# Performance work log

Hardware: AMD Instinct MI355X
Metric: run time of the kernel (lower is better)

The kernel has to match this reference:

```python
import jax, jax.numpy as jnp
import numpy as np

N = 50000      # nodes
E = 800000     # edges
IN = 128       # in_feats
HID = 16       # h_feats (per head)
HEADS = 8      # num_heads layer 1
CLS = 40       # num_classes
NEG_SLOPE = 0.2


def setup_inputs() -> dict:
    key = jax.random.key(0)
    ks = jax.random.split(key, 12)
    s = lambda fan: np.float32(1.0 / np.sqrt(fan))
    return {
        "features": jax.random.normal(ks[0], (N, IN), jnp.float32),
        "edge_src": jax.random.randint(ks[1], (E,), 0, N, dtype=jnp.int32),
        "edge_dst": jax.random.randint(ks[2], (E,), 0, N, dtype=jnp.int32),
        # layer 1 params
        "W1": jax.random.normal(ks[3], (IN, HEADS * HID), jnp.float32) * s(IN),
        "al1": jax.random.normal(ks[4], (HEADS, HID), jnp.float32) * s(HID),
        "ar1": jax.random.normal(ks[5], (HEADS, HID), jnp.float32) * s(HID),
        "b1": jnp.zeros((HEADS * HID,), jnp.float32),
        # layer 2 params (1 head)
        "W2": jax.random.normal(ks[6], (HEADS * HID, CLS), jnp.float32) * s(HEADS * HID),
        "al2": jax.random.normal(ks[7], (1, CLS), jnp.float32) * s(CLS),
        "ar2": jax.random.normal(ks[8], (1, CLS), jnp.float32) * s(CLS),
        "b2": jnp.zeros((CLS,), jnp.float32),
    }


def gat_conv(x, W, al, ar, b, src, dst, heads, out_dim):
    # x: [N, F_in] -> feat: [N, H, D]
    feat = (x @ W).reshape(-1, heads, out_dim)
    el = (feat * al).sum(-1)                      # [N, H]
    er = (feat * ar).sum(-1)                      # [N, H]
    e = jax.nn.leaky_relu(el[src] + er[dst], NEG_SLOPE)  # [E, H]
    # segment softmax over destination neighborhoods
    emax = jax.ops.segment_max(e, dst, num_segments=N)   # [N, H]
    emax = jnp.where(jnp.isfinite(emax), emax, jnp.float32(0.0))
    ee = jnp.exp(e - emax[dst])                   # [E, H]
    denom = jax.ops.segment_sum(ee, dst, num_segments=N)
    alpha = ee / (denom[dst] + jnp.float32(1e-9)) # [E, H]
    msg = alpha[:, :, None] * feat[src]           # [E, H, D]
    out = jax.ops.segment_sum(msg, dst, num_segments=N)  # [N, H, D]
    return out + b.reshape(1, heads, out_dim)


def reference(features, edge_src, edge_dst, W1, al1, ar1, b1, W2, al2, ar2, b2):
    h = jax.nn.elu(gat_conv(features, W1, al1, ar1, b1, edge_src, edge_dst, HEADS, HID))
    h = h.reshape(N, HEADS * HID)                 # flatten(1)
    out = gat_conv(h, W2, al2, ar2, b2, edge_src, edge_dst, 1, CLS)
    return out.mean(axis=1)                       # [N, CLS]
```

## Files before the change

kernel.cpp:

```cpp
#include <hip/hip_runtime.h>
#include <hip/hip_bf16.h>

#define N_NODES 50000
#define N_EDGES 800000
#define IN_F    128
#define HID     16
#define HEADS   8
#define F1      128
#define CLS     40
#define CLSP    64
#define NEG     0.2f
#define NEG_INF (-__builtin_inff())
#define SWEEPS      8
#define SWEEP_RANGE 6250
#define STRIDE      96

typedef __bf16 bf16x8 __attribute__((ext_vector_type(8)));
typedef float  f32x4  __attribute__((ext_vector_type(4)));
typedef float  f32x2  __attribute__((ext_vector_type(2)));

__device__ __forceinline__ float leaky(float v) { return v >= 0.0f ? v : NEG * v; }
__device__ __forceinline__ f32x2 unpk(unsigned u) {
    f32x2 r;
    r.x = __uint_as_float(u << 16);
    r.y = __uint_as_float(u & 0xffff0000u);
    return r;
}

__global__ void setup_kernel(const float* __restrict__ W1, const float* __restrict__ W2,
                             __bf16* __restrict__ w1t, __bf16* __restrict__ w2t,
                             int* __restrict__ cursor) {
    int i = blockIdx.x * blockDim.x + threadIdx.x;
    if (i < N_NODES) cursor[i] = 0;
    if (i < 128 * 128) {
        int n = i >> 7, k = i & 127;
        w1t[i] = (__bf16)W1[k * 128 + n];
    }
    if (i < CLSP * 128) {
        int n = i >> 7, k = i & 127;
        w2t[i] = (n < CLS) ? (__bf16)W2[k * CLS + n] : (__bf16)0.0f;
    }
}

__global__ void scatter_kernel(const int* __restrict__ src, const int* __restrict__ dst,
                               int* __restrict__ cursor, int* __restrict__ srcs_sorted) {
    const int BPS = (N_EDGES + 255) / 256;
    int sweep = blockIdx.x / BPS;
    int e = (blockIdx.x - sweep * BPS) * 256 + threadIdx.x;
    if (e >= N_EDGES) return;
    int d = dst[e];
    int lo = sweep * SWEEP_RANGE;
    if (d < lo || d >= lo + SWEEP_RANGE) return;
    int pos = d * STRIDE + atomicAdd(&cursor[d], 1);
    srcs_sorted[pos] = src[e];
}

__global__ __launch_bounds__(256) void gemm1_mfma(const float* __restrict__ A,
                                                  const __bf16* __restrict__ Wt,
                                                  const float* __restrict__ al1,
                                                  const float* __restrict__ ar1,
                                                  __bf16* __restrict__ outb,
                                                  float* __restrict__ el,
                                                  float* __restrict__ er) {
    int wave = threadIdx.x >> 6, lane = threadIdx.x & 63;
    int m0 = blockIdx.x * 64 + wave * 16;
    int c = lane & 15;
    int row = m0 + c;
    int rowc = row < N_NODES ? row : N_NODES - 1;
    int ko = (lane >> 4) * 8;

    f32x4 acc[8];
    #pragma unroll
    for (int t = 0; t < 8; ++t)
        #pragma unroll
        for (int r = 0; r < 4; ++r) acc[t][r] = 0.f;

    for (int ks = 0; ks < 128; ks += 32) {
        const float* ap = A + (size_t)rowc * 128 + ks + ko;
        float4 u = *(const float4*)ap;
        float4 v = *(const float4*)(ap + 4);
        bf16x8 a;
        a[0] = (__bf16)u.x; a[1] = (__bf16)u.y; a[2] = (__bf16)u.z; a[3] = (__bf16)u.w;
        a[4] = (__bf16)v.x; a[5] = (__bf16)v.y; a[6] = (__bf16)v.z; a[7] = (__bf16)v.w;
        #pragma unroll
        for (int t = 0; t < 8; ++t) {
            bf16x8 b = *(const bf16x8*)(Wt + (size_t)(t * 16 + c) * 128 + ks + ko);
            acc[t] = __builtin_amdgcn_mfma_f32_16x16x32_bf16(a, b, acc[t], 0, 0, 0);
        }
    }
    int rbase = m0 + (lane >> 4) * 4;
    #pragma unroll
    for (int t = 0; t < 8; ++t) {
        int gcol = t * 16 + c;
        #pragma unroll
        for (int r = 0; r < 4; ++r) {
            int grow = rbase + r;
            if (grow < N_NODES) outb[(size_t)grow * 128 + gcol] = (__bf16)acc[t][r];
        }
    }
    #pragma unroll
    for (int t = 0; t < 8; ++t) {
        float alv = al1[t * 16 + c];
        float arv = ar1[t * 16 + c];
        float pe[4], pr[4];
        #pragma unroll
        for (int r = 0; r < 4; ++r) { pe[r] = acc[t][r] * alv; pr[r] = acc[t][r] * arv; }
        #pragma unroll
        for (int mask = 1; mask <= 8; mask <<= 1) {
            #pragma unroll
            for (int r = 0; r < 4; ++r) {
                pe[r] += __shfl_xor(pe[r], mask, 64);
                pr[r] += __shfl_xor(pr[r], mask, 64);
            }
        }
        if (c == 0) {
            #pragma unroll
            for (int r = 0; r < 4; ++r) {
                int grow = rbase + r;
                if (grow < N_NODES) {
                    el[grow * 8 + t] = pe[r];
                    er[grow * 8 + t] = pr[r];
                }
            }
        }
    }
}

__global__ __launch_bounds__(256) void gemm2_mfma(const __bf16* __restrict__ A,
                                                  const __bf16* __restrict__ Wt,
                                                  const float* __restrict__ al2,
                                                  const float* __restrict__ ar2,
                                                  __bf16* __restrict__ out,
                                                  float* __restrict__ el,
                                                  float* __restrict__ er) {
    int wave = threadIdx.x >> 6, lane = threadIdx.x & 63;
    int m0 = blockIdx.x * 64 + wave * 16;
    int c = lane & 15;
    int row = m0 + c;
    int rowc = row < N_NODES ? row : N_NODES - 1;
    int ko = (lane >> 4) * 8;

    f32x4 acc[4];
    #pragma unroll
    for (int t = 0; t < 4; ++t)
        #pragma unroll
        for (int r = 0; r < 4; ++r) acc[t][r] = 0.f;

    for (int ks = 0; ks < 128; ks += 32) {
        bf16x8 a = *(const bf16x8*)(A + (size_t)rowc * 128 + ks + ko);
        #pragma unroll
        for (int t = 0; t < 4; ++t) {
            bf16x8 b = *(const bf16x8*)(Wt + (size_t)(t * 16 + c) * 128 + ks + ko);
            acc[t] = __builtin_amdgcn_mfma_f32_16x16x32_bf16(a, b, acc[t], 0, 0, 0);
        }
    }
    int rbase = m0 + (lane >> 4) * 4;
    #pragma unroll
    for (int t = 0; t < 4; ++t) {
        int gcol = t * 16 + c;
        #pragma unroll
        for (int r = 0; r < 4; ++r) {
            int grow = rbase + r;
            if (grow < N_NODES) out[(size_t)grow * CLSP + gcol] = (__bf16)acc[t][r];
        }
    }
    float pe[4] = {0.f, 0.f, 0.f, 0.f}, pr[4] = {0.f, 0.f, 0.f, 0.f};
    #pragma unroll
    for (int t = 0; t < 3; ++t) {
        int idx = t * 16 + c;
        float alv = (idx < CLS) ? al2[idx] : 0.f;
        float arv = (idx < CLS) ? ar2[idx] : 0.f;
        #pragma unroll
        for (int r = 0; r < 4; ++r) { pe[r] += acc[t][r] * alv; pr[r] += acc[t][r] * arv; }
    }
    #pragma unroll
    for (int mask = 1; mask <= 8; mask <<= 1) {
        #pragma unroll
        for (int r = 0; r < 4; ++r) {
            pe[r] += __shfl_xor(pe[r], mask, 64);
            pr[r] += __shfl_xor(pr[r], mask, 64);
        }
    }
    if (c == 0) {
        #pragma unroll
        for (int r = 0; r < 4; ++r) {
            int grow = rbase + r;
            if (grow < N_NODES) { el[grow] = pe[r]; er[grow] = pr[r]; }
        }
    }
}

__global__ __launch_bounds__(256) void gat1_fused(const int* __restrict__ degs,
                                                  const int* __restrict__ srcs,
                                                  const float* __restrict__ el,
                                                  const float* __restrict__ er,
                                                  const __bf16* __restrict__ feat1b,
                                                  const float* __restrict__ b1,
                                                  __bf16* __restrict__ hbufb) {
    __shared__ float a_lds[4][64 * 8];
    __shared__ int   s_lds[4][64];
    int wave = threadIdx.x >> 6;
    int lane = threadIdx.x & 63;
    int d = blockIdx.x * 4 + wave;
    int off = d * STRIDE;
    int deg = degs[d];

    int h = lane & 7, slot = lane >> 3;
    int q = lane >> 4, fg = lane & 15, hd = fg >> 1;
    float er_d = er[d * 8 + h];

    f32x2 accv[4];
    #pragma unroll
    for (int j = 0; j < 4; ++j) { accv[j].x = 0.f; accv[j].y = 0.f; }

    bool fast = (deg <= 64);
    if (fast) {
        int nit = (deg + 7) >> 3;
        float sc[8];
        int sreg[8];
        float m = NEG_INF;
        #pragma unroll
        for (int it = 0; it < 8; ++it) {
            float v = NEG_INF;
            int e = it * 8 + slot;
            if (it < nit && e < deg) {
                sreg[it] = srcs[off + e];
                v = leaky(el[sreg[it] * 8 + h] + er_d);
            }
            sc[it] = v;
            m = fmaxf(m, v);
        }
        float l = 0.f;
        #pragma unroll
        for (int it = 0; it < 8; ++it)
            l += (sc[it] == NEG_INF) ? 0.f : __expf(sc[it] - m);
        #pragma unroll
        for (int mask = 8; mask <= 32; mask <<= 1) {
            float m2 = __shfl_xor(m, mask, 64);
            float l2 = __shfl_xor(l, mask, 64);
            float mn = fmaxf(m, m2);
            float f1 = (m  == NEG_INF) ? 0.f : __expf(m - mn);
            float f2 = (m2 == NEG_INF) ? 0.f : __expf(m2 - mn);
            l = l * f1 + l2 * f2;
            m = mn;
        }
        float inv_l = 1.f / (l + 1e-9f);
        #pragma unroll
        for (int it = 0; it < 8; ++it) {
            int e = it * 8 + slot;
            if (it < nit && e < deg) {
                a_lds[wave][e * 8 + h] = __expf(sc[it] - m) * inv_l;
                if (h == 0) s_lds[wave][e] = sreg[it];
            }
        }
    }
    __syncthreads();

    if (fast) {
        int ng = (deg + 3) >> 2;
        #pragma unroll 4
        for (int g = 0; g < ng; ++g) {
            int k = g * 4 + q;
            float a = 0.f;
            int se = 0;
            if (k < deg) {
                a = a_lds[wave][k * 8 + hd];
                se = s_lds[wave][k];
            }
            uint4 p = *(const uint4*)(feat1b + (size_t)se * F1 + fg * 8);
            f32x2 av; av.x = a; av.y = a;
            accv[0] += av * unpk(p.x);
            accv[1] += av * unpk(p.y);
            accv[2] += av * unpk(p.z);
            accv[3] += av * unpk(p.w);
        }
    } else {
        float m = NEG_INF, l = 0.f;
        for (int base = 0; base < deg; base += 8) {
            int e = base + slot;
            float v = NEG_INF;
            if (e < deg) {
                int s = srcs[off + e];
                v = leaky(el[s * 8 + h] + er_d);
            }
            float mn = fmaxf(m, v);
            float f1 = (m == NEG_INF) ? 0.f : __expf(m - mn);
            float f2 = (v == NEG_INF) ? 0.f : __expf(v - mn);
            l = l * f1 + f2;
            m = mn;
        }
        #pragma unroll
        for (int mask = 8; mask <= 32; mask <<= 1) {
            float m2 = __shfl_xor(m, mask, 64);
            float l2 = __shfl_xor(l, mask, 64);
            float mn = fmaxf(m, m2);
            float f1 = (m  == NEG_INF) ? 0.f : __expf(m - mn);
            float f2 = (m2 == NEG_INF) ? 0.f : __expf(m2 - mn);
            l = l * f1 + l2 * f2;
            m = mn;
        }
        float inv_l = 1.f / (l + 1e-9f);

        for (int base = 0; base < deg; base += 8) {
            int e = base + slot;
            float alpha = 0.f;
            int s = 0;
            if (e < deg) {
                s = srcs[off + e];
                float v = leaky(el[s * 8 + h] + er_d);
                alpha = __expf(v - m) * inv_l;
            }
            #pragma unroll
            for (int sub = 0; sub < 2; ++sub) {
                int k = sub * 4 + q;
                float a  = __shfl(alpha, k * 8 + hd, 64);
                int   se = __shfl(s,     k * 8,      64);
                uint4 p = *(const uint4*)(feat1b + (size_t)se * F1 + fg * 8);
                f32x2 av; av.x = a; av.y = a;
                accv[0] += av * unpk(p.x);
                accv[1] += av * unpk(p.y);
                accv[2] += av * unpk(p.z);
                accv[3] += av * unpk(p.w);
            }
        }
    }

    float acc[8];
    #pragma unroll
    for (int j = 0; j < 4; ++j) { acc[2 * j] = accv[j].x; acc[2 * j + 1] = accv[j].y; }
    #pragma unroll
    for (int i = 0; i < 8; ++i) {
        acc[i] += __shfl_xor(acc[i], 16, 64);
        acc[i] += __shfl_xor(acc[i], 32, 64);
    }
    if (q == 0) {
        bf16x8 o;
        #pragma unroll
        for (int i = 0; i < 8; ++i) {
            float v = acc[i] + b1[fg * 8 + i];
            v = v > 0.f ? v : expm1f(v);
            o[i] = (__bf16)v;
        }
        *(bf16x8*)(hbufb + (size_t)d * F1 + fg * 8) = o;
    }
}

__global__ __launch_bounds__(256) void gat2_fused(const int* __restrict__ degs,
                                                  const int* __restrict__ srcs,
                                                  const float* __restrict__ el,
                                                  const float* __restrict__ er,
                                                  const __bf16* __restrict__ feat2p,
                                                  const float* __restrict__ b2,
                                                  float* __restrict__ out) {
    __shared__ float a_lds[4][64];
    __shared__ int   s_lds[4][64];
    int wave = threadIdx.x >> 6;
    int lane = threadIdx.x & 63;
    int d = blockIdx.x * 4 + wave;
    int off = d * STRIDE;
    int deg = degs[d];

    float er_d = er[d];
    int q  = lane >> 4;
    int cg = lane & 15;
    f32x2 accv[2];
    accv[0].x = 0.f; accv[0].y = 0.f; accv[1].x = 0.f; accv[1].y = 0.f;

    bool fast = (deg <= 64);
    if (fast) {
        float sc = NEG_INF;
        int s0 = 0;
        if (lane < deg) {
            s0 = srcs[off + lane];
            sc = leaky(el[s0] + er_d);
        }
        float m = sc, l = (sc == NEG_INF) ? 0.f : 1.f;
        #pragma unroll
        for (int mask = 1; mask <= 32; mask <<= 1) {
            float m2 = __shfl_xor(m, mask, 64);
            float l2 = __shfl_xor(l, mask, 64);
            float mn = fmaxf(m, m2);
            float f1 = (m  == NEG_INF) ? 0.f : __expf(m - mn);
            float f2 = (m2 == NEG_INF) ? 0.f : __expf(m2 - mn);
            l = l * f1 + l2 * f2;
            m = mn;
        }
        float inv_l = 1.f / (l + 1e-9f);
        if (lane < deg) {
            a_lds[wave][lane] = __expf(sc - m) * inv_l;
            s_lds[wave][lane] = s0;
        }
    }
    __syncthreads();

    if (fast) {
        int ng = (deg + 3) >> 2;
        #pragma unroll 4
        for (int g = 0; g < ng; ++g) {
            int k = g * 4 + q;
            float a = 0.f;
            int se = 0;
            if (k < deg) {
                a = a_lds[wave][k];
                se = s_lds[wave][k];
            }
            uint2 p = *(const uint2*)(feat2p + (size_t)se * CLSP + cg * 4);
            f32x2 av; av.x = a; av.y = a;
            accv[0] += av * unpk(p.x);
            accv[1] += av * unpk(p.y);
        }
    } else {
        float m = NEG_INF, l = 0.f;
        for (int base = 0; base < deg; base += 64) {
            int e = base + lane;
            float sc = NEG_INF;
            if (e < deg) {
                int s = srcs[off + e];
                sc = leaky(el[s] + er_d);
            }
            float mn = fmaxf(m, sc);
            float f1 = (m  == NEG_INF) ? 0.f : __expf(m - mn);
            float f2 = (sc == NEG_INF) ? 0.f : __expf(sc - mn);
            l = l * f1 + f2;
            m = mn;
        }
        #pragma unroll
        for (int mask = 1; mask <= 32; mask <<= 1) {
            float m2 = __shfl_xor(m, mask, 64);
            float l2 = __shfl_xor(l, mask, 64);
            float mn = fmaxf(m, m2);
            float f1 = (m  == NEG_INF) ? 0.f : __expf(m - mn);
            float f2 = (m2 == NEG_INF) ? 0.f : __expf(m2 - mn);
            l = l * f1 + l2 * f2;
            m = mn;
        }
        float inv_l = 1.f / (l + 1e-9f);

        for (int base = 0; base < deg; base += 64) {
            int e = base + lane;
            float alpha = 0.f;
            int s = 0;
            if (e < deg) {
                s = srcs[off + e];
                float sc = leaky(el[s] + er_d);
                alpha = __expf(sc - m) * inv_l;
            }
            int kmax = min(64, deg - base);
            int nsub = (kmax + 3) >> 2;
            for (int sub = 0; sub < nsub; ++sub) {
                int k = sub * 4 + q;
                float a  = __shfl(alpha, k, 64);
                int   se = __shfl(s,     k, 64);
                uint2 p = *(const uint2*)(feat2p + (size_t)se * CLSP + cg * 4);
                f32x2 av; av.x = a; av.y = a;
                accv[0] += av * unpk(p.x);
                accv[1] += av * unpk(p.y);
            }
        }
    }

    float acc[4];
    acc[0] = accv[0].x; acc[1] = accv[0].y; acc[2] = accv[1].x; acc[3] = accv[1].y;
    #pragma unroll
    for (int i = 0; i < 4; ++i) {
        acc[i] += __shfl_xor(acc[i], 16, 64);
        acc[i] += __shfl_xor(acc[i], 32, 64);
    }
    if (lane < 10) {
        float4 o;
        o.x = acc[0] + b2[cg * 4 + 0];
        o.y = acc[1] + b2[cg * 4 + 1];
        o.z = acc[2] + b2[cg * 4 + 2];
        o.w = acc[3] + b2[cg * 4 + 3];
        *(float4*)(out + (size_t)d * CLS + cg * 4) = o;
    }
}

extern "C" void kernel_launch(void* const* d_in, const int* in_sizes, int n_in,
                              void* d_out, int out_size, void* d_ws, size_t ws_size,
                              hipStream_t stream) {
    const float* features = (const float*)d_in[0];
    const int*   esrc     = (const int*)d_in[1];
    const int*   edst     = (const int*)d_in[2];
    const float* W1       = (const float*)d_in[3];
    const float* al1      = (const float*)d_in[4];
    const float* ar1      = (const float*)d_in[5];
    const float* b1       = (const float*)d_in[6];
    const float* W2       = (const float*)d_in[7];
    const float* al2      = (const float*)d_in[8];
    const float* ar2      = (const float*)d_in[9];
    const float* b2       = (const float*)d_in[10];
    float* out = (float*)d_out;

    float* ws = (float*)d_ws;
    float*  el1    = ws;
    float*  er1    = ws + 400000;
    float*  el2    = ws + 800000;
    float*  er2    = ws + 850000;
    int*    cursor = (int*)(ws + 900000);
    int*    srcs   = (int*)(ws + 950000);
    __bf16* feat1b = (__bf16*)(ws + 5750000);
    __bf16* hbufb  = (__bf16*)(ws + 8950000);
    __bf16* feat2p = (__bf16*)(ws + 12150000);
    __bf16* w1t    = (__bf16*)(ws + 13750000);
    __bf16* w2t    = (__bf16*)(ws + 13760000);

    const int B = 256;
    const int BPS = (N_EDGES + 255) / 256;

    setup_kernel<<<(N_NODES + B - 1) / B, B, 0, stream>>>(W1, W2, w1t, w2t, cursor);
    scatter_kernel<<<SWEEPS * BPS, B, 0, stream>>>(esrc, edst, cursor, srcs);

    gemm1_mfma<<<(N_NODES + 63) / 64, 256, 0, stream>>>(features, w1t, al1, ar1,
                                                        feat1b, el1, er1);
    gat1_fused<<<N_NODES / 4, B, 0, stream>>>(cursor, srcs, el1, er1, feat1b, b1, hbufb);

    gemm2_mfma<<<(N_NODES + 63) / 64, 256, 0, stream>>>(hbufb, w2t, al2, ar2,
                                                        feat2p, el2, er2);
    gat2_fused<<<N_NODES / 4, B, 0, stream>>>(cursor, srcs, el2, er2, feat2p, b2, out);
}
```

Baseline: 270.0 us.

## Prefetch neighbor feature rows before softmax and drop block barrier in GAT aggregation

In both GAT layers the fast path now issues all neighbor feature-row gathers into registers before computing the attention softmax, so memory latency overlaps the score computation. The block-wide barrier goes away: layer 1 keeps a per-wave LDS buffer only for alpha, and layer 2 broadcasts alpha and source indices with wave shuffles instead of LDS. The fast-path threshold drops from degree 64 to 32 to bound the prefetch registers, which sends more nodes to the slower online-softmax path. Register pressure rises and occupancy may fall.

```diff
diff --git a/kernel.cpp b/kernel.cpp
--- a/kernel.cpp
+++ b/kernel.cpp
@@ -197,8 +197,7 @@
                                                   const __bf16* __restrict__ feat1b,
                                                   const float* __restrict__ b1,
                                                   __bf16* __restrict__ hbufb) {
-    __shared__ float a_lds[4][64 * 8];
-    __shared__ int   s_lds[4][64];
+    __shared__ float a_lds[4][32 * 8];
     int wave = threadIdx.x >> 6;
     int lane = threadIdx.x & 63;
     int d = blockIdx.x * 4 + wave;
@@ -213,26 +212,35 @@
     #pragma unroll
     for (int j = 0; j < 4; ++j) { accv[j].x = 0.f; accv[j].y = 0.f; }
 
-    bool fast = (deg <= 64);
+    bool fast = (deg <= 32);
     if (fast) {
+        int ng = (deg + 3) >> 2;
+        uint4 pref[8];
+        #pragma unroll
+        for (int g = 0; g < 8; ++g) {
+            if (g < ng) {
+                int k = g * 4 + q;
+                int se = (k < deg) ? srcs[off + k] : 0;
+                pref[g] = *(const uint4*)(feat1b + (size_t)se * F1 + fg * 8);
+            }
+        }
         int nit = (deg + 7) >> 3;
-        float sc[8];
-        int sreg[8];
+        float sc[4];
         float m = NEG_INF;
         #pragma unroll
-        for (int it = 0; it < 8; ++it) {
+        for (int it = 0; it < 4; ++it) {
             float v = NEG_INF;
             int e = it * 8 + slot;
             if (it < nit && e < deg) {
-                sreg[it] = srcs[off + e];
-                v = leaky(el[sreg[it] * 8 + h] + er_d);
+                int s = srcs[off + e];
+                v = leaky(el[s * 8 + h] + er_d);
             }
             sc[it] = v;
             m = fmaxf(m, v);
         }
         float l = 0.f;
         #pragma unroll
-        for (int it = 0; it < 8; ++it)
+        for (int it = 0; it < 4; ++it)
             l += (sc[it] == NEG_INF) ? 0.f : __expf(sc[it] - m);
         #pragma unroll
         for (int mask = 8; mask <= 32; mask <<= 1) {
@@ -246,33 +254,22 @@
         }
         float inv_l = 1.f / (l + 1e-9f);
         #pragma unroll
-        for (int it = 0; it < 8; ++it) {
+        for (int it = 0; it < 4; ++it) {
             int e = it * 8 + slot;
-            if (it < nit && e < deg) {
+            if (it < nit && e < deg)
                 a_lds[wave][e * 8 + h] = __expf(sc[it] - m) * inv_l;
-                if (h == 0) s_lds[wave][e] = sreg[it];
-            }
-        }
-    }
-    __syncthreads();
-
-    if (fast) {
-        int ng = (deg + 3) >> 2;
-        #pragma unroll 4
-        for (int g = 0; g < ng; ++g) {
-            int k = g * 4 + q;
-            float a = 0.f;
-            int se = 0;
-            if (k < deg) {
-                a = a_lds[wave][k * 8 + hd];
-                se = s_lds[wave][k];
-            }
-            uint4 p = *(const uint4*)(feat1b + (size_t)se * F1 + fg * 8);
-            f32x2 av; av.x = a; av.y = a;
-            accv[0] += av * unpk(p.x);
-            accv[1] += av * unpk(p.y);
-            accv[2] += av * unpk(p.z);
-            accv[3] += av * unpk(p.w);
+        }
+        #pragma unroll
+        for (int g = 0; g < 8; ++g) {
+            if (g < ng) {
+                int k = g * 4 + q;
+                float a = (k < deg) ? a_lds[wave][k * 8 + hd] : 0.f;
+                f32x2 av; av.x = a; av.y = a;
+                accv[0] += av * unpk(pref[g].x);
+                accv[1] += av * unpk(pref[g].y);
+                accv[2] += av * unpk(pref[g].z);
+                accv[3] += av * unpk(pref[g].w);
+            }
         }
     } else {
         float m = NEG_INF, l = 0.f;
@@ -352,8 +349,6 @@
                                                   const __bf16* __restrict__ feat2p,
                                                   const float* __restrict__ b2,
                                                   float* __restrict__ out) {
-    __shared__ float a_lds[4][64];
-    __shared__ int   s_lds[4][64];
     int wave = threadIdx.x >> 6;
     int lane = threadIdx.x & 63;
     int d = blockIdx.x * 4 + wave;
@@ -366,13 +361,23 @@
     f32x2 accv[2];
     accv[0].x = 0.f; accv[0].y = 0.f; accv[1].x = 0.f; accv[1].y = 0.f;
 
-    bool fast = (deg <= 64);
+    bool fast = (deg <= 32);
     if (fast) {
         float sc = NEG_INF;
         int s0 = 0;
         if (lane < deg) {
             s0 = srcs[off + lane];
             sc = leaky(el[s0] + er_d);
+        }
+        int ng = (deg + 3) >> 2;
+        uint2 pref[8];
+        #pragma unroll
+        for (int g = 0; g < 8; ++g) {
+            if (g < ng) {
+                int k = g * 4 + q;
+                int se = __shfl(s0, k, 64);
+                pref[g] = *(const uint2*)(feat2p + (size_t)se * CLSP + cg * 4);
+            }
         }
         float m = sc, l = (sc == NEG_INF) ? 0.f : 1.f;
         #pragma unroll
@@ -386,28 +391,16 @@
             m = mn;
         }
         float inv_l = 1.f / (l + 1e-9f);
-        if (lane < deg) {
-            a_lds[wave][lane] = __expf(sc - m) * inv_l;
-            s_lds[wave][lane] = s0;
-        }
-    }
-    __syncthreads();
-
-    if (fast) {
-        int ng = (deg + 3) >> 2;
-        #pragma unroll 4
-        for (int g = 0; g < ng; ++g) {
-            int k = g * 4 + q;
-            float a = 0.f;
-            int se = 0;
-            if (k < deg) {
-                a = a_lds[wave][k];
-                se = s_lds[wave][k];
-            }
-            uint2 p = *(const uint2*)(feat2p + (size_t)se * CLSP + cg * 4);
-            f32x2 av; av.x = a; av.y = a;
-            accv[0] += av * unpk(p.x);
-            accv[1] += av * unpk(p.y);
+        float alpha = (sc == NEG_INF) ? 0.f : __expf(sc - m) * inv_l;
+        #pragma unroll
+        for (int g = 0; g < 8; ++g) {
+            if (g < ng) {
+                int k = g * 4 + q;
+                float a = __shfl(alpha, k, 64);
+                f32x2 av; av.x = a; av.y = a;
+                accv[0] += av * unpk(pref[g].x);
+                accv[1] += av * unpk(pref[g].y);
+            }
         }
     } else {
         float m = NEG_INF, l = 0.f;
```

Measured after the change: 271.9 us. No clear change (+0.7%).
